# Kernel tuning notes

Hardware: AMD Instinct MI355X
Metric: run time of the kernel (lower is better)

The kernel has to match this reference:

```python
import jax, jax.numpy as jnp
import numpy as np

N, E = 40000, 640000
D, H, DK = 128, 8, 16   # out_dim, n_heads, d_k = D // H
T, R = 3, 4             # num node types, num relation types


def setup_inputs() -> dict:
    key = jax.random.key(0)
    ks = jax.random.split(key, 16)
    glorot = lambda k, shape, fan: jax.random.normal(k, shape, jnp.float32) * np.sqrt(2.0 / fan)
    inp = {
        'node_inp': jax.random.normal(ks[0], (N, D), jnp.float32),
        'node_type': jax.random.randint(ks[1], (N,), 0, T),
        'edge_index': jax.random.randint(ks[2], (2, E), 0, N),
        'edge_type': jax.random.randint(ks[3], (E,), 0, R),
        'node_position': jax.random.randint(ks[4], (N,), 0, N),
        # per-node-type Linear weights, stored [T, in, out] (y = x @ W + b)
        'Kw': glorot(ks[5], (T, D, D), 2 * D), 'Kb': jnp.zeros((T, D), jnp.float32),
        'Qw': glorot(ks[6], (T, D, D), 2 * D), 'Qb': jnp.zeros((T, D), jnp.float32),
        'Vw': glorot(ks[7], (T, D, D), 2 * D), 'Vb': jnp.zeros((T, D), jnp.float32),
        'Aw': glorot(ks[8], (T, D, D), 2 * D), 'Ab': jnp.zeros((T, D), jnp.float32),
        'relation_pri': jnp.ones((T, R, T, H), jnp.float32),
        'relation_att': glorot(ks[9], (R, H, DK, DK), 2 * DK),
        'relation_msg': glorot(ks[10], (R, H, DK, DK), 2 * DK),
        'relation_s2u': glorot(ks[11], (D, D), 2 * D),
        'skip': jnp.ones((T,), jnp.float32),
    }
    return inp


def reference(node_inp, node_type, edge_index, edge_type, node_position,
              Kw, Kb, Qw, Qb, Vw, Vb, Aw, Ab,
              relation_pri, relation_att, relation_msg, relation_s2u, skip):
    n = node_inp.shape[0]
    src, tgt = edge_index[0], edge_index[1]  # j (source), i (target)
    ar = jnp.arange(n)

    # per-type K/Q/V projections for every node: [T, N, D], then select own type
    k_all = jnp.einsum('nd,tdo->tno', node_inp, Kw) + Kb[:, None, :]
    q_all = jnp.einsum('nd,tdo->tno', node_inp, Qw) + Qb[:, None, :]
    v_all = jnp.einsum('nd,tdo->tno', node_inp, Vw) + Vb[:, None, :]
    k_node = k_all[node_type, ar]
    q_node = q_all[node_type, ar]
    v_node = v_all[node_type, ar]

    k_j = k_node[src].reshape(-1, H, DK)
    v_j = v_node[src].reshape(-1, H, DK)
    q_i = q_node[tgt].reshape(-1, H, DK)

    # per-relation attention / message transforms (select per edge relation)
    k_t = jnp.zeros_like(k_j)
    v_t = jnp.zeros_like(v_j)
    for r in range(R):
        sel = (edge_type == r)[:, None, None]
        k_t = jnp.where(sel, jnp.einsum('ehd,hdf->ehf', k_j, relation_att[r]), k_t)
        v_t = jnp.where(sel, jnp.einsum('ehd,hdf->ehf', v_j, relation_msg[r]), v_t)

    st, tt = node_type[src], node_type[tgt]
    pri = relation_pri[tt, edge_type, st]                       # [E, H]
    att_raw = (q_i * k_t).sum(-1) * pri / np.sqrt(DK)           # [E, H]

    # scatter-softmax over edges sharing the same target node
    m = jax.ops.segment_max(att_raw, tgt, num_segments=n)
    m = jnp.where(jnp.isfinite(m), m, 0.0)
    ex = jnp.exp(att_raw - m[tgt])
    den = jax.ops.segment_sum(ex, tgt, num_segments=n)
    att = ex / (den[tgt] + 1e-16)

    msg = (v_t * att[:, :, None]).reshape(-1, D)
    aggr = jax.ops.segment_sum(msg, tgt, num_segments=n)        # scatter-add

    # speaker information: edges with edge_type==0, message from target rep to source index
    sp_in = v_all[1][tgt]                                       # v_linears[1](node_inp[edge_index_i])
    sp_msg = sp_in @ relation_s2u                               # [E, D]
    drop_idx = jnp.where(edge_type == 0, src, n)                # out-of-range -> dropped
    speaker_info = jnp.zeros((n, D), node_inp.dtype).at[drop_idx].set(sp_msg, mode='drop')

    aggr = jax.nn.gelu(aggr + speaker_info, approximate=False)

    # target-specific aggregation with per-type learnable skip (dropout=eval identity)
    a_all = jnp.einsum('no,tof->tnf', aggr, Aw) + Ab[:, None, :]
    a_node = a_all[node_type, ar]
    alpha = jax.nn.sigmoid(skip)[node_type][:, None]
    return a_node * alpha + node_inp * (1.0 - alpha)
```

## Files before the change

kernel.cpp:

```cpp
#include <hip/hip_runtime.h>
#include <hip/hip_bf16.h>
#include <math.h>

#define ND 128
#define NH 8
#define DKK 16
#define NT 3
#define NR 4
#define NB 8
#define NMAT 12
#define SCB 4096

typedef unsigned short ushort_t;
typedef __bf16 bf16_t;
typedef bf16_t bf16x8 __attribute__((ext_vector_type(8)));
typedef float f32x4 __attribute__((ext_vector_type(4)));

__device__ __forceinline__ float bf2f(unsigned short u) {
    union { unsigned int i; float f; } v; v.i = ((unsigned int)u) << 16; return v.f;
}
__device__ __forceinline__ unsigned short f2bf(float f) {
    union { float f; unsigned int i; } v; v.f = f;
    unsigned int x = v.i;
    unsigned int lsb = (x >> 16) & 1u;
    x += 0x7fffu + lsb;
    return (unsigned short)(x >> 16);
}
__device__ __forceinline__ unsigned int pk2(float a, float b) {
    return (unsigned int)f2bf(a) | ((unsigned int)f2bf(b) << 16);
}
__device__ __forceinline__ void load_bf8(const ushort_t* p, float* o) {
    uint4 u = *reinterpret_cast<const uint4*>(p);
    o[0]=bf2f(u.x & 0xffff); o[1]=bf2f(u.x >> 16);
    o[2]=bf2f(u.y & 0xffff); o[3]=bf2f(u.y >> 16);
    o[4]=bf2f(u.z & 0xffff); o[5]=bf2f(u.z >> 16);
    o[6]=bf2f(u.w & 0xffff); o[7]=bf2f(u.w >> 16);
}
__device__ __forceinline__ bf16x8 as_bf16x8(uint4 u) {
    union { uint4 u; bf16x8 v; } c; c.u = u; return c.v;
}


__global__ void k_zero(int n, int* offs, int* winner) {
    int i = blockIdx.x * 256 + threadIdx.x;
    if (i < n) { offs[i] = 0; winner[i] = -1; }
}

__global__ void k_count(int e, const int* src, const int* tgt, const int* etype,
                        int* offs, int* winner, int* rank) {
    int i = blockIdx.x * 256 + threadIdx.x;
    if (i < e) {
        rank[i] = atomicAdd(&offs[tgt[i]], 1);
        if (etype[i] == 0) atomicMax(&winner[src[i]], i);
    }
}


__global__ void k_scanA(int n, const int* offs, const int* ntype, int* bsum4) {
    __shared__ int red[256];
    __shared__ int tr[256][3];
    int b = blockIdx.x, tid = threadIdx.x;
    int base = b * SCB + tid * 16;
    int s = 0, c0 = 0, c1 = 0, c2 = 0;
    #pragma unroll
    for (int i = 0; i < 16; i++) {
        int idx = base + i;
        if (idx < n) {
            s += offs[idx];
            int t = ntype[idx];
            c0 += (t == 0); c1 += (t == 1); c2 += (t == 2);
        }
    }
    red[tid] = s; tr[tid][0] = c0; tr[tid][1] = c1; tr[tid][2] = c2;
    __syncthreads();
    for (int d = 128; d > 0; d >>= 1) {
        if (tid < d) {
            red[tid] += red[tid + d];
            tr[tid][0] += tr[tid + d][0];
            tr[tid][1] += tr[tid + d][1];
            tr[tid][2] += tr[tid + d][2];
        }
        __syncthreads();
    }
    if (tid == 0) {
        bsum4[b * 4]     = red[0];
        bsum4[b * 4 + 1] = tr[0][0];
        bsum4[b * 4 + 2] = tr[0][1];
        bsum4[b * 4 + 3] = tr[0][2];
    }
}

__global__ void k_scanB(int nb, const int* bsum4, int* boff4, int* tcnt, int* tstart) {
    if (threadIdx.x == 0) {
        int run = 0, r0 = 0, r1 = 0, r2 = 0;
        for (int b = 0; b < nb; b++) {
            boff4[b * 4]     = run;
            boff4[b * 4 + 1] = r0;
            boff4[b * 4 + 2] = r1;
            boff4[b * 4 + 3] = r2;
            run += bsum4[b * 4];
            r0  += bsum4[b * 4 + 1];
            r1  += bsum4[b * 4 + 2];
            r2  += bsum4[b * 4 + 3];
        }
        tcnt[0] = r0; tcnt[1] = r1; tcnt[2] = r2;
        tstart[0] = 0; tstart[1] = r0; tstart[2] = r0 + r1;
    }
}

__global__ void k_scanC(int n, int* offs, const int* ntype, const int* boff4,
                        const int* tstart, int* order) {
    __shared__ int red[256];
    __shared__ int tr[256][3];
    int b = blockIdx.x, tid = threadIdx.x;
    int base = b * SCB + tid * 16;
    int v[16]; signed char ty[16];
    int s = 0, c0 = 0, c1 = 0, c2 = 0;
    #pragma unroll
    for (int i = 0; i < 16; i++) {
        int idx = base + i;
        v[i] = (idx < n) ? offs[idx] : 0;
        s += v[i];
        int t = (idx < n) ? ntype[idx] : -1;
        ty[i] = (signed char)t;
        c0 += (t == 0); c1 += (t == 1); c2 += (t == 2);
    }
    red[tid] = s; tr[tid][0] = c0; tr[tid][1] = c1; tr[tid][2] = c2;
    __syncthreads();
    for (int d = 1; d < 256; d <<= 1) {
        int vv = (tid >= d) ? red[tid - d] : 0;
        int w0 = (tid >= d) ? tr[tid - d][0] : 0;
        int w1 = (tid >= d) ? tr[tid - d][1] : 0;
        int w2 = (tid >= d) ? tr[tid - d][2] : 0;
        __syncthreads();
        red[tid] += vv; tr[tid][0] += w0; tr[tid][1] += w1; tr[tid][2] += w2;
        __syncthreads();
    }
    int run = boff4[b * 4] + red[tid] - s;
    int p0 = tstart[0] + boff4[b * 4 + 1] + tr[tid][0] - c0;
    int p1 = tstart[1] + boff4[b * 4 + 2] + tr[tid][1] - c1;
    int p2 = tstart[2] + boff4[b * 4 + 3] + tr[tid][2] - c2;
    #pragma unroll
    for (int i = 0; i < 16; i++) {
        int idx = base + i;
        if (idx < n) {
            offs[idx] = run; run += v[i];
            int t = ty[i];
            if (t == 0)      order[p0++] = idx;
            else if (t == 1) order[p1++] = idx;
            else             order[p2++] = idx;
        }
    }
    if (base <= n && n < base + 16) offs[n] = run;
}

__global__ void k_scatter(int e, const int* src, const int* tgt, const int* etype,
                          const int* ntype, const int* offs, const int* rank,
                          int* eord, int mode) {
    int i = blockIdx.x * 256 + threadIdx.x;
    if (i < e) {
        int p = offs[tgt[i]] + rank[i];
        if (mode) {
            int s = src[i];
            eord[p] = (s * NR + etype[i]) | (ntype[s] << 28);
        } else {
            eord[p] = i;
        }
    }
}


__global__ void k_pack(const float* Qw, const float* Qb, const float* Kw, const float* Kb,
                       const float* Vw, const float* Vb, const float* Aw, const float* Ab,
                       const float* s2u, const float* r_att, const float* r_msg,
                       ushort_t* Wall, float* bcat) {
    int blk = blockIdx.x;
    int kb = blk & 3;
    int c = (blk >> 2) & 7;
    int tm = blk >> 5;
    int m = tm % NMAT, t = tm / NMAT;
    int lane = threadIdx.x;
    int nn = c * 16 + (lane & 15);
    int quad = lane >> 4;
    int k0 = kb * 32 + quad * 8;
    ushort_t* dst = Wall + (size_t)blk * 512 + lane * 8;

    if (m == 0 || m == 5 || m == 10 || m == 11) {
        const float* W; const float* B;
        if (m == 0)       { W = Qw + (size_t)t * ND * ND; B = Qb + t * ND; }
        else if (m == 5)  { W = Vw + (size_t)ND * ND;     B = Vb + ND; }
        else if (m == 10) { W = Aw + (size_t)t * ND * ND; B = Ab + t * ND; }
        else              { W = s2u;                      B = nullptr; }
        #pragma unroll
        for (int j = 0; j < 8; j++) dst[j] = f2bf(W[(size_t)(k0 + j) * ND + nn]);
        if (kb == 0 && quad == 0)
            bcat[(t * NMAT + m) * ND + nn] = B ? B[nn] : 0.f;
    } else {
        int r = (m <= 4) ? (m - 1) : (m - 6);
        const float* W0 = (m <= 4) ? Kw : Vw;
        const float* B0 = (m <= 4) ? Kb : Vb;
        const float* Wr = (m <= 4) ? r_att : r_msg;
        int h = c, f = lane & 15;
        float wcol[16];
        #pragma unroll
        for (int jj = 0; jj < 16; jj++)
            wcol[jj] = Wr[(((size_t)r * NH + h) * DKK + jj) * DKK + f];
        #pragma unroll
        for (int j = 0; j < 8; j++) {
            const float* row = W0 + ((size_t)t * ND + (k0 + j)) * ND + h * DKK;
            float s = 0.f;
            #pragma unroll
            for (int jj = 0; jj < 16; jj++) s += row[jj] * wcol[jj];
            dst[j] = f2bf(s);
        }
        if (kb == 0 && quad == 0) {
            const float* brow = B0 + t * ND + h * DKK;
            float sb = 0.f;
            #pragma unroll
            for (int jj = 0; jj < 16; jj++) sb += brow[jj] * wcol[jj];
            bcat[(t * NMAT + m) * ND + nn] = sb;
        }
    }
}

__global__ void __launch_bounds__(256) k_projm(
    int n, const float* x_in, const int* order,
    const int* tcnt, const int* tstart,
    const ushort_t* Wall, const float* bcat,
    int m0, int nm,
    ushort_t* out_qn, ushort_t* out_kt, ushort_t* out_v1, ushort_t* out_vt)
{
    __shared__ __align__(16) ushort_t xs[4096];
    __shared__ int nodes[32];
    int b = blockIdx.x;
    int nb0 = (tcnt[0] + 31) >> 5, nb1 = (tcnt[1] + 31) >> 5, nb2 = (tcnt[2] + 31) >> 5;
    int t, lb;
    if (b < nb0)                  { t = 0; lb = b; }
    else if (b < nb0 + nb1)       { t = 1; lb = b - nb0; }
    else if (b < nb0 + nb1 + nb2) { t = 2; lb = b - nb0 - nb1; }
    else return;
    int segoff = lb * 32;
    int cnt = min(32, tcnt[t] - segoff);
    int segbase = tstart[t] + segoff;
    int tid = threadIdx.x;
    if (tid < 32) nodes[tid] = (tid < cnt) ? order[segbase + tid] : -1;
    __syncthreads();
    {
        int row = tid >> 3;
        int d0 = (tid & 7) * 16;
        int rt = row >> 4, rl = row & 15;
        int kb = d0 >> 5, q0 = (d0 >> 3) & 3;
        uint4 c0, c1;
        if (row < cnt) {
            const float4* xp4 = (const float4*)(x_in + (size_t)nodes[row] * ND + d0);
            float4 a = xp4[0], b2 = xp4[1], c2 = xp4[2], d4 = xp4[3];
            c0.x = pk2(a.x, a.y);   c0.y = pk2(a.z, a.w);
            c0.z = pk2(b2.x, b2.y); c0.w = pk2(b2.z, b2.w);
            c1.x = pk2(c2.x, c2.y); c1.y = pk2(c2.z, c2.w);
            c1.z = pk2(d4.x, d4.y); c1.w = pk2(d4.z, d4.w);
        } else {
            c0.x = c0.y = c0.z = c0.w = 0u;
            c1 = c0;
        }
        *(uint4*)&xs[((rt * 4 + kb) * 64 + q0 * 16 + rl) * 8]       = c0;
        *(uint4*)&xs[((rt * 4 + kb) * 64 + (q0 + 1) * 16 + rl) * 8] = c1;
    }
    __syncthreads();

    int w = tid >> 6, lane = tid & 63;
    int rt = w & 1;
    bf16x8 afr[4];
    #pragma unroll
    for (int kb = 0; kb < 4; kb++)
        afr[kb] = as_bf16x8(*(const uint4*)&xs[((rt * 4 + kb) * 64 + lane) * 8]);
    int nct = nm * 8;
    for (int ct = (w >> 1); ct < nct; ct += 2) {
        int m = m0 + (ct >> 3), c = ct & 7;
        const uint4* bp = (const uint4*)(Wall + ((((size_t)t * NMAT + m) * 8 + c) * 4) * 512);
        f32x4 acc = {0.f, 0.f, 0.f, 0.f};
        #pragma unroll
        for (int kb = 0; kb < 4; kb++) {
            bf16x8 bfr = as_bf16x8(bp[kb * 64 + lane]);
            acc = __builtin_amdgcn_mfma_f32_16x16x32_bf16(afr[kb], bfr, acc, 0, 0, 0);
        }
        int col = c * 16 + (lane & 15);
        float bias = bcat[(t * NMAT + m) * ND + col];
        int rbase = rt * 16 + (lane >> 4) * 4;
        #pragma unroll
        for (int r = 0; r < 4; r++) {
            int grow = rbase + r;
            if (grow >= cnt) continue;
            int node = nodes[grow];
            ushort_t val = f2bf(acc[r] + bias);
            if (m == 0)       out_qn[(size_t)node * ND + col] = val;
            else if (m <= 4)  out_kt[((size_t)node * NR + (m - 1)) * ND + col] = val;
            else if (m == 5)  out_v1[(size_t)node * ND + col] = val;
            else              out_vt[((size_t)node * NR + (m - 6)) * ND + col] = val;
        }
    }
}

__global__ void __launch_bounds__(256) k_projall(
    int n, const float* x_in, const int* order,
    const int* tcnt, const int* tstart,
    const ushort_t* Wall, const float* bcat,
    ushort_t* out_qn, ushort_t* out_kt, ushort_t* out_v1, ushort_t* out_vt)
{
    __shared__ __align__(16) ushort_t xs[4096];
    __shared__ int nodes[32];
    int b = blockIdx.x;
    int nb0 = (tcnt[0] + 31) >> 5, nb1 = (tcnt[1] + 31) >> 5, nb2 = (tcnt[2] + 31) >> 5;
    int t, lb;
    if (b < nb0)                  { t = 0; lb = b; }
    else if (b < nb0 + nb1)       { t = 1; lb = b - nb0; }
    else if (b < nb0 + nb1 + nb2) { t = 2; lb = b - nb0 - nb1; }
    else return;
    int segoff = lb * 32;
    int cnt = min(32, tcnt[t] - segoff);
    int segbase = tstart[t] + segoff;
    int tid = threadIdx.x;
    if (tid < 32) nodes[tid] = (tid < cnt) ? order[segbase + tid] : -1;
    __syncthreads();
    {
        int row = tid >> 3;
        int d0 = (tid & 7) * 16;
        int rt = row >> 4, rl = row & 15;
        int kb = d0 >> 5, q0 = (d0 >> 3) & 3;
        uint4 c0, c1;
        if (row < cnt) {
            const float4* xp4 = (const float4*)(x_in + (size_t)nodes[row] * ND + d0);
            float4 a = xp4[0], b2 = xp4[1], c2 = xp4[2], d4 = xp4[3];
            c0.x = pk2(a.x, a.y);   c0.y = pk2(a.z, a.w);
            c0.z = pk2(b2.x, b2.y); c0.w = pk2(b2.z, b2.w);
            c1.x = pk2(c2.x, c2.y); c1.y = pk2(c2.z, c2.w);
            c1.z = pk2(d4.x, d4.y); c1.w = pk2(d4.z, d4.w);
        } else {
            c0.x = c0.y = c0.z = c0.w = 0u;
            c1 = c0;
        }
        *(uint4*)&xs[((rt * 4 + kb) * 64 + q0 * 16 + rl) * 8]       = c0;
        *(uint4*)&xs[((rt * 4 + kb) * 64 + (q0 + 1) * 16 + rl) * 8] = c1;
    }
    __syncthreads();

    int w = tid >> 6, lane = tid & 63;
    int rt = w & 1;
    bf16x8 afr[4];
    #pragma unroll
    for (int kb = 0; kb < 4; kb++)
        afr[kb] = as_bf16x8(*(const uint4*)&xs[((rt * 4 + kb) * 64 + lane) * 8]);
    for (int ct = (w >> 1); ct < 80; ct += 2) {
        int m = ct >> 3, c = ct & 7;
        const uint4* bp = (const uint4*)(Wall + ((((size_t)t * NMAT + m) * 8 + c) * 4) * 512);
        f32x4 acc = {0.f, 0.f, 0.f, 0.f};
        #pragma unroll
        for (int kb = 0; kb < 4; kb++) {
            bf16x8 bfr = as_bf16x8(bp[kb * 64 + lane]);
            acc = __builtin_amdgcn_mfma_f32_16x16x32_bf16(afr[kb], bfr, acc, 0, 0, 0);
        }
        int col = c * 16 + (lane & 15);
        float bias = bcat[(t * NMAT + m) * ND + col];
        int rbase = rt * 16 + (lane >> 4) * 4;
        #pragma unroll
        for (int r = 0; r < 4; r++) {
            int grow = rbase + r;
            if (grow >= cnt) continue;
            int node = nodes[grow];
            ushort_t val = f2bf(acc[r] + bias);
            if (m == 0)       out_qn[(size_t)node * ND + col] = val;
            else if (m <= 4)  out_kt[((size_t)node * NR + (m - 1)) * ND + col] = val;
            else if (m == 5)  out_v1[(size_t)node * ND + col] = val;
            else              out_vt[((size_t)node * NR + (m - 6)) * ND + col] = val;
        }
    }
}

__global__ void __launch_bounds__(256) k_flash(
    int n, const int* off, const int* srp, const int* ntype,
    const ushort_t* qn, const ushort_t* kt, const ushort_t* vt,
    const float* r_pri, float* aggr)
{
    int wv = threadIdx.x >> 6, lane = threadIdx.x & 63;
    int i = blockIdx.x * 4 + wv;
    if (i >= n) return;
    int h = lane & 7, slot = lane >> 3;
    int hA = lane >> 3;
    int tt = ntype[i];
    float qf[16];
    load_bf8(qn + (size_t)i * ND + h * DKK, qf);
    load_bf8(qn + (size_t)i * ND + h * DKK + 8, qf + 8);
    const float* prib = r_pri + (size_t)(tt * NR * NT) * NH + h;
    int d0 = off[i], d1 = off[i + 1];
    float m = -3.0e38f, den = 0.f;
    float acc0 = 0.f, acc1 = 0.f;
    for (int p0 = d0; p0 < d1; p0 += 8) {
        int p = p0 + slot;
        bool live = (p < d1);
        int sp = live ? srp[p] : 0;
        int sr = sp & 0x0fffffff;
        int st = ((unsigned int)sp) >> 28;
        int r = sr & (NR - 1);
        float kf[16];
        const ushort_t* kp = kt + (size_t)sr * ND + h * DKK;
        load_bf8(kp, kf);
        load_bf8(kp + 8, kf + 8);
        float a = 0.f;
        #pragma unroll
        for (int f = 0; f < 16; f++) a += qf[f] * kf[f];
        float pri = prib[(r * NT + st) * NH];
        float logit = fminf(fmaxf(a * pri * 0.25f, -1.0e4f), 1.0e4f);
        if (!live) logit = -3.0e38f;
        float cm = logit;
        #pragma unroll
        for (int d = 8; d < 64; d <<= 1) cm = fmaxf(cm, __shfl_xor(cm, d, 64));
        float mnew = fmaxf(m, cm);
        float w = live ? expf(logit - mnew) : 0.f;
        float ws = w;
        #pragma unroll
        for (int d = 8; d < 64; d <<= 1) ws += __shfl_xor(ws, d, 64);
        float scale = expf(m - mnew);
        den = den * scale + ws;
        m = mnew;
        float scaleA = __shfl(scale, hA, 64);
        acc0 *= scaleA; acc1 *= scaleA;
        #pragma unroll
        for (int s = 0; s < 8; s++) {
            if (p0 + s < d1) {
                int srcl = s * 8 + hA;
                int srb  = __shfl(sr, srcl, 64);
                float wb = __shfl(w, srcl, 64);
                unsigned int u = *reinterpret_cast<const unsigned int*>(
                    vt + (size_t)srb * ND + lane * 2);
                acc0 += wb * bf2f(u & 0xffff);
                acc1 += wb * bf2f(u >> 16);
            }
        }
    }
    float denA = __shfl(den, hA, 64);
    float inv = 1.f / (denA + 1e-16f);
    float2 o; o.x = acc0 * inv; o.y = acc1 * inv;
    *reinterpret_cast<float2*>(aggr + (size_t)i * ND + lane * 2) = o;
}

__global__ void __launch_bounds__(256) k_sfinal(
    int n, const float* x_in, const int* order, const int* tcnt, const int* tstart,
    const int* winner, const int* tgt, const ushort_t* v1b,
    const ushort_t* Wall, const float* bcat, const float* skip,
    const float* aggr, float* out)
{
    __shared__ __align__(16) float xf[32 * 132];
    __shared__ __align__(16) ushort_t xs[4096];
    __shared__ int nodes[32];
    __shared__ int wsrc[32];
    int b = blockIdx.x;
    int nb0 = (tcnt[0] + 31) >> 5, nb1 = (tcnt[1] + 31) >> 5, nb2 = (tcnt[2] + 31) >> 5;
    int t, lb;
    if (b < nb0)                  { t = 0; lb = b; }
    else if (b < nb0 + nb1)       { t = 1; lb = b - nb0; }
    else if (b < nb0 + nb1 + nb2) { t = 2; lb = b - nb0 - nb1; }
    else return;
    int segoff = lb * 32;
    int cnt = min(32, tcnt[t] - segoff);
    int segbase = tstart[t] + segoff;
    int tid = threadIdx.x;
    if (tid < 32) {
        int nd = (tid < cnt) ? order[segbase + tid] : -1;
        nodes[tid] = nd;
        int wi = (nd >= 0) ? winner[nd] : -1;
        wsrc[tid] = (wi >= 0) ? tgt[wi] : -1;
    }
    __syncthreads();
    {
        int row = tid >> 3;
        int d0 = (tid & 7) * 16;
        int rt = row >> 4, rl = row & 15;
        int kb = d0 >> 5, q0 = (d0 >> 3) & 3;
        uint4 c0, c1;
        int s = (row < cnt) ? wsrc[row] : -1;
        if (s >= 0) {
            const uint4* vp = (const uint4*)(v1b + (size_t)s * ND + d0);
            c0 = vp[0]; c1 = vp[1];
        } else { c0.x = c0.y = c0.z = c0.w = 0u; c1 = c0; }
        *(uint4*)&xs[((rt * 4 + kb) * 64 + q0 * 16 + rl) * 8]       = c0;
        *(uint4*)&xs[((rt * 4 + kb) * 64 + (q0 + 1) * 16 + rl) * 8] = c1;
    }
    __syncthreads();
    int w = tid >> 6, lane = tid & 63;
    int rt = w & 1;
    {
        bf16x8 afr[4];
        #pragma unroll
        for (int kb = 0; kb < 4; kb++)
            afr[kb] = as_bf16x8(*(const uint4*)&xs[((rt * 4 + kb) * 64 + lane) * 8]);
        for (int ct = (w >> 1); ct < 8; ct += 2) {
            const uint4* bp = (const uint4*)(Wall + (((size_t)11 * 8 + ct) * 4) * 512);
            f32x4 acc = {0.f, 0.f, 0.f, 0.f};
            #pragma unroll
            for (int kb = 0; kb < 4; kb++) {
                bf16x8 bfr = as_bf16x8(bp[kb * 64 + lane]);
                acc = __builtin_amdgcn_mfma_f32_16x16x32_bf16(afr[kb], bfr, acc, 0, 0, 0);
            }
            int col = ct * 16 + (lane & 15);
            int rbase = rt * 16 + (lane >> 4) * 4;
            #pragma unroll
            for (int r = 0; r < 4; r++) {
// ... 231 lines not shown
    float den = 0.f;
    for (int p = d0; p < d1; p++) den += expf(att[(size_t)sorted[p] * NH + h] - mref);
    mb[id] = mh;
    db[id] = den;
}

__global__ void k_norm(int e, const int* tgt, const ushort_t* mb, const float* db, float* att) {
    int id = blockIdx.x * 256 + threadIdx.x;
    if (id >= e * NH) return;
    int ee = id >> 3, h = id & 7;
    int t = tgt[ee];
    float w = expf(att[id] - bf2f(mb[t * NH + h])) / (db[t * NH + h] + 1e-16f);
    att[id] = w;
}

__global__ void k_aggr(int n, const int* off, const int* sorted, const int* src, const int* etype,
                       const ushort_t* vn, const float* r_msg, const float* att, float* aggr) {
    int wv = threadIdx.x >> 6, lane = threadIdx.x & 63;
    int i = blockIdx.x * 4 + wv;
    if (i >= n) return;
    int h = lane >> 3, f0 = (lane & 7) * 2;
    int d0 = off[i], d1 = off[i + 1];
    float acc0 = 0.f, acc1 = 0.f;
    for (int p = d0; p < d1; p++) {
        int ee = sorted[p];
        int s = src[ee], r = etype[ee];
        float w = att[(size_t)ee * NH + h];
        float vj[16];
        load_bf8(vn + (size_t)s * ND + h * DKK, vj);
        load_bf8(vn + (size_t)s * ND + h * DKK + 8, vj + 8);
        const float* Wm = r_msg + (size_t)(r * NH + h) * DKK * DKK + f0;
        float a0 = 0.f, a1 = 0.f;
        #pragma unroll
        for (int d = 0; d < 16; d++) {
            a0 += vj[d] * Wm[d * 16];
            a1 += vj[d] * Wm[d * 16 + 1];
        }
        acc0 += w * a0; acc1 += w * a1;
    }
    aggr[(size_t)i * ND + h * DKK + f0]     = acc0;
    aggr[(size_t)i * ND + h * DKK + f0 + 1] = acc1;
}

__global__ void k_spk(int n, const int* winner, const int* tgt, const ushort_t* v1,
                      const float* s2u, float* aggr) {
    __shared__ float xs[NB][ND];
    __shared__ int wn[NB];
    int tid = threadIdx.x;
    int base = blockIdx.x * NB;
    int cnt = min(NB, n - base);
    if (tid < cnt) wn[tid] = winner[base + tid];
    __syncthreads();
    for (int j = 0; j < cnt; j++) {
        int w = wn[j];
        xs[j][tid] = (w >= 0) ? bf2f(v1[(size_t)tgt[w] * ND + tid]) : 0.f;
    }
    __syncthreads();
    float acc[NB];
    #pragma unroll
    for (int j = 0; j < NB; j++) acc[j] = 0.f;
    const float* Wp = s2u + tid;
    for (int d = 0; d < ND; d++) {
        float w = Wp[(size_t)d * ND];
        #pragma unroll
        for (int j = 0; j < NB; j++) acc[j] += xs[j][d] * w;
    }
    for (int j = 0; j < cnt; j++) {
        size_t idx = (size_t)(base + j) * ND + tid;
        float g = aggr[idx] + acc[j];
        g = 0.5f * g * (1.f + erff(g * 0.70710678118f));
        aggr[idx] = g;
    }
}

__global__ void k_final(int n, const float* x_in, const int* ntype, const int* order,
                        const float* Aw, const float* Ab, const float* skip,
                        const float* aggr, float* out) {
    __shared__ float xs[NB][ND];
    __shared__ int nodes[NB];
    __shared__ int types[NB];
    int tid = threadIdx.x;
    int base = blockIdx.x * NB;
    int cnt = min(NB, n - base);
    if (tid < cnt) { int nd = order[base + tid]; nodes[tid] = nd; types[tid] = ntype[nd]; }
    __syncthreads();
    for (int j = 0; j < cnt; j++) xs[j][tid] = aggr[(size_t)nodes[j] * ND + tid];
    __syncthreads();
    bool uni = (types[0] == types[cnt - 1]);
    if (uni) {
        int t = types[0];
        float bias = Ab[t * ND + tid];
        float acc[NB];
        #pragma unroll
        for (int j = 0; j < NB; j++) acc[j] = bias;
        const float* Wp = Aw + (size_t)t * ND * ND + tid;
        for (int d = 0; d < ND; d++) {
            float w = Wp[(size_t)d * ND];
            #pragma unroll
            for (int j = 0; j < NB; j++) acc[j] += xs[j][d] * w;
        }
        float alpha = 1.f / (1.f + expf(-skip[t]));
        for (int j = 0; j < cnt; j++) {
            float xin = x_in[(size_t)nodes[j] * ND + tid];
            out[(size_t)nodes[j] * ND + tid] = acc[j] * alpha + xin * (1.f - alpha);
        }
    } else {
        for (int j = 0; j < cnt; j++) {
            int t = types[j];
            float acc = Ab[t * ND + tid];
            const float* Wp = Aw + (size_t)t * ND * ND + tid;
            for (int d = 0; d < ND; d++) acc += xs[j][d] * Wp[(size_t)d * ND];
            float alpha = 1.f / (1.f + expf(-skip[t]));
            float xin = x_in[(size_t)nodes[j] * ND + tid];
            out[(size_t)nodes[j] * ND + tid] = acc * alpha + xin * (1.f - alpha);
        }
    }
}

extern "C" void kernel_launch(void* const* d_in, const int* in_sizes, int n_in,
                              void* d_out, int out_size, void* d_ws, size_t ws_size,
                              hipStream_t stream) {
    const float* node_inp = (const float*)d_in[0];
    const int* node_type  = (const int*)d_in[1];
    const int* edge_index = (const int*)d_in[2];
    const int* edge_type  = (const int*)d_in[3];
    const float* Kw = (const float*)d_in[5];
    const float* Kb = (const float*)d_in[6];
    const float* Qw = (const float*)d_in[7];
    const float* Qb = (const float*)d_in[8];
    const float* Vw = (const float*)d_in[9];
    const float* Vb = (const float*)d_in[10];
    const float* Aw = (const float*)d_in[11];
    const float* Ab = (const float*)d_in[12];
    const float* r_pri = (const float*)d_in[13];
    const float* r_att = (const float*)d_in[14];
    const float* r_msg = (const float*)d_in[15];
    const float* s2u   = (const float*)d_in[16];
    const float* skip  = (const float*)d_in[17];

    int n = in_sizes[1];
    int e = in_sizes[3];
    const int* srcp = edge_index;
    const int* tgtp = edge_index + e;

    char* wsp = (char*)d_ws;
    size_t woff = 0;
    auto alloc = [&](size_t b) { void* p = wsp + woff; woff += (b + 255) & ~(size_t)255; return p; };

    int* offs     = (int*)alloc((size_t)(n + 1) * 4);
    int* winner   = (int*)alloc((size_t)n * 4);
    int* order    = (int*)alloc((size_t)n * 4);
    int* tcnt     = (int*)alloc(16);
    int* tstart   = (int*)alloc(16);
    int* bsum4    = (int*)alloc(4096);
    int* boff4    = (int*)alloc(4096);
    int* eord     = (int*)alloc((size_t)e * 4);
    ushort_t* mb  = (ushort_t*)alloc((size_t)n * NH * 2);
    float* db     = (float*)alloc((size_t)n * NH * 4);
    ushort_t* v1b = (ushort_t*)alloc((size_t)n * ND * 2);
    float* att    = (float*)alloc((size_t)e * NH * 4);
    size_t commonEnd = woff;

    int* rank = (int*)att;

    woff = commonEnd;
    ushort_t* WallB = (ushort_t*)alloc((size_t)NT * NMAT * 8 * 4 * 512 * 2);
    float* bcatB    = (float*)alloc((size_t)NT * NMAT * ND * 4);
    char* F         = (char*)alloc((size_t)n * 1536);
    size_t fastEnd = woff;

    woff = commonEnd;
    ushort_t* WallA = (ushort_t*)alloc((size_t)NT * NMAT * 8 * 4 * 512 * 2);
    float* bcatA    = (float*)alloc((size_t)NT * NMAT * ND * 4);
    ushort_t* qnA   = (ushort_t*)alloc((size_t)n * ND * 2);
    ushort_t* ktA   = (ushort_t*)alloc((size_t)n * NR * ND * 2);
    ushort_t* vtA   = (ushort_t*)alloc((size_t)n * NR * ND * 2);
    size_t tierAEnd = woff;
    float* aggrA = (float*)att;

    int gn = (n + 255) / 256;
    int ge = (e + 255) / 256;
    int nbscan = n / SCB + 1;
    int gproj = (n + 31) / 32 + NT;

    int tierA = (ws_size >= tierAEnd) && ((size_t)e * NH >= (size_t)n * ND);
    int fast  = (ws_size >= fastEnd);

    k_zero<<<gn, 256, 0, stream>>>(n, offs, winner);
    k_count<<<ge, 256, 0, stream>>>(e, srcp, tgtp, edge_type, offs, winner, rank);
    k_scanA<<<nbscan, 256, 0, stream>>>(n, offs, node_type, bsum4);
    k_scanB<<<1, 64, 0, stream>>>(nbscan, bsum4, boff4, tcnt, tstart);
    k_scanC<<<nbscan, 256, 0, stream>>>(n, offs, node_type, boff4, tstart, order);
    k_scatter<<<ge, 256, 0, stream>>>(e, srcp, tgtp, edge_type, node_type, offs, rank,
                                      eord, (tierA || fast) ? 1 : 0);

    if (tierA) {
        k_pack<<<NT * NMAT * 8 * 4, 64, 0, stream>>>(Qw, Qb, Kw, Kb, Vw, Vb, Aw, Ab,
                                                     s2u, r_att, r_msg, WallA, bcatA);
        k_projall<<<gproj, 256, 0, stream>>>(n, node_inp, order, tcnt, tstart, WallA, bcatA,
                                             qnA, ktA, v1b, vtA);
        k_flash<<<(n + 3) / 4, 256, 0, stream>>>(n, offs, eord, node_type,
                                                 qnA, ktA, vtA, r_pri, aggrA);
        k_sfinal<<<gproj, 256, 0, stream>>>(n, node_inp, order, tcnt, tstart,
                                            winner, tgtp, v1b, WallA, bcatA, skip,
                                            aggrA, (float*)d_out);
    } else if (fast) {
        ushort_t* qn  = (ushort_t*)F;
        ushort_t* kt  = (ushort_t*)(F + (size_t)n * 256);
        ushort_t* vt  = (ushort_t*)F;
        float* aggr   = (float*)(F + (size_t)n * 1024);

        k_pack<<<NT * NMAT * 8 * 4, 64, 0, stream>>>(Qw, Qb, Kw, Kb, Vw, Vb, Aw, Ab,
                                                     s2u, r_att, r_msg, WallB, bcatB);
        k_projm<<<gproj, 256, 0, stream>>>(n, node_inp, order, tcnt, tstart, WallB, bcatB,
                                           0, 6, qn, kt, v1b, (ushort_t*)nullptr);
        k_attmd<<<(n + 3) / 4, 256, 0, stream>>>(n, offs, eord, node_type,
                                                 qn, kt, r_pri, att, mb, db);
        k_projm<<<gproj, 256, 0, stream>>>(n, node_inp, order, tcnt, tstart, WallB, bcatB,
                                           6, 4, (ushort_t*)nullptr, (ushort_t*)nullptr,
                                           (ushort_t*)nullptr, vt);
        k_aggr_fast<<<(n + 3) / 4, 256, 0, stream>>>(n, offs, eord, vt, att, mb, db, aggr);
        k_sfinal<<<gproj, 256, 0, stream>>>(n, node_inp, order, tcnt, tstart,
                                            winner, tgtp, v1b, WallB, bcatB, skip,
                                            aggr, (float*)d_out);
    } else {
        woff = commonEnd;
        ushort_t* vn  = (ushort_t*)alloc((size_t)n * ND * 2);
        char* regA    = (char*)alloc((size_t)n * ND * 2 * 2);
        ushort_t* kn  = (ushort_t*)regA;
        ushort_t* qn  = (ushort_t*)(regA + (size_t)n * ND * 2);
        float* aggr   = (float*)regA;

        k_proj<<<(n + NB - 1) / NB, 128, 0, stream>>>(n, node_inp, node_type, order,
                                                      Kw, Kb, Qw, Qb, Vw, Vb, kn, qn, vn, v1b);
        k_att<<<(e * NH + 255) / 256, 256, 0, stream>>>(e, srcp, tgtp, edge_type, node_type,
                                                        kn, qn, r_att, r_pri, att);
        k_mden<<<(n * NH + 255) / 256, 256, 0, stream>>>(n, offs, eord, att, mb, db);
        k_norm<<<(e * NH + 255) / 256, 256, 0, stream>>>(e, tgtp, mb, db, att);
        k_aggr<<<(n + 3) / 4, 256, 0, stream>>>(n, offs, eord, srcp, edge_type, vn, r_msg, att, aggr);
        k_spk<<<(n + NB - 1) / NB, 128, 0, stream>>>(n, winner, tgtp, v1b, s2u, aggr);
        k_final<<<(n + NB - 1) / NB, 128, 0, stream>>>(n, node_inp, node_type, order,
                                                       Aw, Ab, skip, aggr, (float*)d_out);
    }
}
```

Before: 323.8 us.

## Fuse edge counting into projection kernel and split node-type and offset scans

```diff
diff --git a/kernel.cpp b/kernel.cpp
--- a/kernel.cpp
+++ b/kernel.cpp
@@ -47,35 +47,32 @@
 }
 
 __global__ void k_count(int e, const int* src, const int* tgt, const int* etype,
-                        int* offs, int* winner, int* rank) {
+                        int* cnts, int* winner, int* rank) {
     int i = blockIdx.x * 256 + threadIdx.x;
     if (i < e) {
-        rank[i] = atomicAdd(&offs[tgt[i]], 1);
+        rank[i] = atomicAdd(&cnts[tgt[i]], 1);
         if (etype[i] == 0) atomicMax(&winner[src[i]], i);
     }
 }
 
 
-__global__ void k_scanA(int n, const int* offs, const int* ntype, int* bsum4) {
-    __shared__ int red[256];
+__global__ void k_nscanA(int n, const int* ntype, int* nb4) {
     __shared__ int tr[256][3];
     int b = blockIdx.x, tid = threadIdx.x;
     int base = b * SCB + tid * 16;
-    int s = 0, c0 = 0, c1 = 0, c2 = 0;
+    int c0 = 0, c1 = 0, c2 = 0;
     #pragma unroll
     for (int i = 0; i < 16; i++) {
         int idx = base + i;
         if (idx < n) {
-            s += offs[idx];
             int t = ntype[idx];
             c0 += (t == 0); c1 += (t == 1); c2 += (t == 2);
         }
     }
-    red[tid] = s; tr[tid][0] = c0; tr[tid][1] = c1; tr[tid][2] = c2;
+    tr[tid][0] = c0; tr[tid][1] = c1; tr[tid][2] = c2;
     __syncthreads();
     for (int d = 128; d > 0; d >>= 1) {
         if (tid < d) {
-            red[tid] += red[tid + d];
             tr[tid][0] += tr[tid + d][0];
             tr[tid][1] += tr[tid + d][1];
             tr[tid][2] += tr[tid + d][2];
@@ -83,73 +80,119 @@
         __syncthreads();
     }
     if (tid == 0) {
-        bsum4[b * 4]     = red[0];
-        bsum4[b * 4 + 1] = tr[0][0];
-        bsum4[b * 4 + 2] = tr[0][1];
-        bsum4[b * 4 + 3] = tr[0][2];
-    }
-}
-
-__global__ void k_scanB(int nb, const int* bsum4, int* boff4, int* tcnt, int* tstart) {
+        nb4[b * 4]     = tr[0][0];
+        nb4[b * 4 + 1] = tr[0][1];
+        nb4[b * 4 + 2] = tr[0][2];
+    }
+}
+
+__global__ void k_nscanB(int nb, const int* nb4, int* nboff4, int* tcnt, int* tstart) {
     if (threadIdx.x == 0) {
-        int run = 0, r0 = 0, r1 = 0, r2 = 0;
+        int r0 = 0, r1 = 0, r2 = 0;
         for (int b = 0; b < nb; b++) {
-            boff4[b * 4]     = run;
-            boff4[b * 4 + 1] = r0;
-            boff4[b * 4 + 2] = r1;
-            boff4[b * 4 + 3] = r2;
-            run += bsum4[b * 4];
-            r0  += bsum4[b * 4 + 1];
-            r1  += bsum4[b * 4 + 2];
-            r2  += bsum4[b * 4 + 3];
+            nboff4[b * 4]     = r0;
+            nboff4[b * 4 + 1] = r1;
+            nboff4[b * 4 + 2] = r2;
+            r0 += nb4[b * 4];
+            r1 += nb4[b * 4 + 1];
+            r2 += nb4[b * 4 + 2];
         }
         tcnt[0] = r0; tcnt[1] = r1; tcnt[2] = r2;
         tstart[0] = 0; tstart[1] = r0; tstart[2] = r0 + r1;
     }
 }
 
-__global__ void k_scanC(int n, int* offs, const int* ntype, const int* boff4,
-                        const int* tstart, int* order) {
-    __shared__ int red[256];
+__global__ void k_nscanC(int n, const int* ntype, const int* nboff4,
+                         const int* tstart, int* order) {
     __shared__ int tr[256][3];
     int b = blockIdx.x, tid = threadIdx.x;
     int base = b * SCB + tid * 16;
-    int v[16]; signed char ty[16];
-    int s = 0, c0 = 0, c1 = 0, c2 = 0;
+    signed char ty[16];
+    int c0 = 0, c1 = 0, c2 = 0;
+    #pragma unroll
+    for (int i = 0; i < 16; i++) {
+        int idx = base + i;
+        int t = (idx < n) ? ntype[idx] : -1;
+        ty[i] = (signed char)t;
+        c0 += (t == 0); c1 += (t == 1); c2 += (t == 2);
+    }
+    tr[tid][0] = c0; tr[tid][1] = c1; tr[tid][2] = c2;
+    __syncthreads();
+    for (int d = 1; d < 256; d <<= 1) {
+        int w0 = (tid >= d) ? tr[tid - d][0] : 0;
+        int w1 = (tid >= d) ? tr[tid - d][1] : 0;
+        int w2 = (tid >= d) ? tr[tid - d][2] : 0;
+        __syncthreads();
+        tr[tid][0] += w0; tr[tid][1] += w1; tr[tid][2] += w2;
+        __syncthreads();
+    }
+    int p0 = tstart[0] + nboff4[b * 4]     + tr[tid][0] - c0;
+    int p1 = tstart[1] + nboff4[b * 4 + 1] + tr[tid][1] - c1;
+    int p2 = tstart[2] + nboff4[b * 4 + 2] + tr[tid][2] - c2;
+    #pragma unroll
+    for (int i = 0; i < 16; i++) {
+        int idx = base + i;
+        if (idx < n) {
+            int t = ty[i];
+            if (t == 0)      order[p0++] = idx;
+            else if (t == 1) order[p1++] = idx;
+            else             order[p2++] = idx;
+        }
+    }
+}
+
+
+__global__ void k_oscanA(int n, const int* offs, int* ob) {
+    __shared__ int red[256];
+    int b = blockIdx.x, tid = threadIdx.x;
+    int base = b * SCB + tid * 16;
+    int s = 0;
+    #pragma unroll
+    for (int i = 0; i < 16; i++) {
+        int idx = base + i;
+        if (idx < n) s += offs[idx];
+    }
+    red[tid] = s;
+    __syncthreads();
+    for (int d = 128; d > 0; d >>= 1) {
+        if (tid < d) red[tid] += red[tid + d];
+        __syncthreads();
+    }
+    if (tid == 0) ob[b] = red[0];
+}
+
+__global__ void k_oscanB(int nb, const int* ob, int* oboff) {
+    if (threadIdx.x == 0) {
+        int run = 0;
+        for (int b = 0; b < nb; b++) { oboff[b] = run; run += ob[b]; }
+    }
+}
+
+__global__ void k_oscanC(int n, int* offs, const int* oboff) {
+    __shared__ int red[256];
+    int b = blockIdx.x, tid = threadIdx.x;
+    int base = b * SCB + tid * 16;
+    int v[16];
+    int s = 0;
     #pragma unroll
     for (int i = 0; i < 16; i++) {
         int idx = base + i;
         v[i] = (idx < n) ? offs[idx] : 0;
         s += v[i];
-        int t = (idx < n) ? ntype[idx] : -1;
-        ty[i] = (signed char)t;
-        c0 += (t == 0); c1 += (t == 1); c2 += (t == 2);
-    }
-    red[tid] = s; tr[tid][0] = c0; tr[tid][1] = c1; tr[tid][2] = c2;
+    }
+    red[tid] = s;
     __syncthreads();
     for (int d = 1; d < 256; d <<= 1) {
         int vv = (tid >= d) ? red[tid - d] : 0;
-        int w0 = (tid >= d) ? tr[tid - d][0] : 0;
-        int w1 = (tid >= d) ? tr[tid - d][1] : 0;
-        int w2 = (tid >= d) ? tr[tid - d][2] : 0;
         __syncthreads();
-        red[tid] += vv; tr[tid][0] += w0; tr[tid][1] += w1; tr[tid][2] += w2;
+        red[tid] += vv;
         __syncthreads();
     }
-    int run = boff4[b * 4] + red[tid] - s;
-    int p0 = tstart[0] + boff4[b * 4 + 1] + tr[tid][0] - c0;
-    int p1 = tstart[1] + boff4[b * 4 + 2] + tr[tid][1] - c1;
-    int p2 = tstart[2] + boff4[b * 4 + 3] + tr[tid][2] - c2;
+    int run = oboff[b] + red[tid] - s;
     #pragma unroll
     for (int i = 0; i < 16; i++) {
         int idx = base + i;
-        if (idx < n) {
-            offs[idx] = run; run += v[i];
-            int t = ty[i];
-            if (t == 0)      order[p0++] = idx;
-            else if (t == 1) order[p1++] = idx;
-            else             order[p2++] = idx;
-        }
+        if (idx < n) { offs[idx] = run; run += v[i]; }
     }
     if (base <= n && n < base + 16) offs[n] = run;
 }
@@ -219,6 +262,94 @@
             #pragma unroll
             for (int jj = 0; jj < 16; jj++) sb += brow[jj] * wcol[jj];
             bcat[(t * NMAT + m) * ND + nn] = sb;
+        }
+    }
+}
+
+__global__ void __launch_bounds__(256) k_fuse(
+    int n, int e, int gproj, int gtot,
+    const int* src, const int* tgt, const int* etype,
+    int* cnts, int* winner, int* rank,
+    const float* x_in, const int* order, const int* tcnt, const int* tstart,
+    const ushort_t* Wall, const float* bcat,
+    ushort_t* out_qn, ushort_t* out_kt, ushort_t* out_v1, ushort_t* out_vt)
+{
+    __shared__ __align__(16) ushort_t xs[4096];
+    __shared__ int nodes[32];
+    int bid = blockIdx.x;
+    int pb  = (int)(((long long)bid * gproj) / gtot);
+    int pb1 = (int)(((long long)(bid + 1) * gproj) / gtot);
+    if (pb1 == pb) {
+        int i = (bid - pb) * 256 + threadIdx.x;
+        if (i < e) {
+            rank[i] = atomicAdd(&cnts[tgt[i]], 1);
+            if (etype[i] == 0) atomicMax(&winner[src[i]], i);
+        }
+        return;
+    }
+    int b = pb;
+    int nb0 = (tcnt[0] + 31) >> 5, nb1 = (tcnt[1] + 31) >> 5, nb2 = (tcnt[2] + 31) >> 5;
+    int t, lb;
+    if (b < nb0)                  { t = 0; lb = b; }
+    else if (b < nb0 + nb1)       { t = 1; lb = b - nb0; }
+    else if (b < nb0 + nb1 + nb2) { t = 2; lb = b - nb0 - nb1; }
+    else return;
+    int segoff = lb * 32;
+    int cnt = min(32, tcnt[t] - segoff);
+    int segbase = tstart[t] + segoff;
+    int tid = threadIdx.x;
+    if (tid < 32) nodes[tid] = (tid < cnt) ? order[segbase + tid] : -1;
+    __syncthreads();
+    {
+        int row = tid >> 3;
+        int d0 = (tid & 7) * 16;
+        int rt = row >> 4, rl = row & 15;
+        int kb = d0 >> 5, q0 = (d0 >> 3) & 3;
+        uint4 c0, c1;
+        if (row < cnt) {
+            const float4* xp4 = (const float4*)(x_in + (size_t)nodes[row] * ND + d0);
+            float4 a = xp4[0], b2 = xp4[1], c2 = xp4[2], d4 = xp4[3];
+            c0.x = pk2(a.x, a.y);   c0.y = pk2(a.z, a.w);
+            c0.z = pk2(b2.x, b2.y); c0.w = pk2(b2.z, b2.w);
+            c1.x = pk2(c2.x, c2.y); c1.y = pk2(c2.z, c2.w);
+            c1.z = pk2(d4.x, d4.y); c1.w = pk2(d4.z, d4.w);
+        } else {
+            c0.x = c0.y = c0.z = c0.w = 0u;
+            c1 = c0;
+        }
+        *(uint4*)&xs[((rt * 4 + kb) * 64 + q0 * 16 + rl) * 8]       = c0;
+        *(uint4*)&xs[((rt * 4 + kb) * 64 + (q0 + 1) * 16 + rl) * 8] = c1;
+    }
+    __syncthreads();
+
+    int w = tid >> 6, lane = tid & 63;
+    int rt = w & 1;
+    bf16x8 afr[4];
+    #pragma unroll
+    for (int kb = 0; kb < 4; kb++)
+        afr[kb] = as_bf16x8(*(const uint4*)&xs[((rt * 4 + kb) * 64 + lane) * 8]);
+    for (int ct = (w >> 1); ct < 80; ct += 2) {
+        int m = ct >> 3, c = ct & 7;
+        const uint4* bp = (const uint4*)(Wall + ((((size_t)t * NMAT + m) * 8 + c) * 4) * 512);
+        f32x4 acc = {0.f, 0.f, 0.f, 0.f};
+        #pragma unroll
+        for (int kb = 0; kb < 4; kb++) {
+            bf16x8 bfr = as_bf16x8(bp[kb * 64 + lane]);
+            acc = __builtin_amdgcn_mfma_f32_16x16x32_bf16(afr[kb], bfr, acc, 0, 0, 0);
+        }
+        int col = c * 16 + (lane & 15);
+        float bias = bcat[(t * NMAT + m) * ND + col];
+        int rbase = rt * 16 + (lane >> 4) * 4;
+        #pragma unroll
+        for (int r = 0; r < 4; r++) {
+            int grow = rbase + r;
+            if (grow >= cnt) continue;
+            int node = nodes[grow];
+            ushort_t val = f2bf(acc[r] + bias);
+            if (m == 0)       out_qn[(size_t)node * ND + col] = val;
+            else if (m <= 4)  out_kt[((size_t)node * NR + (m - 1)) * ND + col] = val;
+            else if (m == 5)  out_v1[(size_t)node * ND + col] = val;
+            else              out_vt[((size_t)node * NR + (m - 6)) * ND + col] = val;
         }
     }
 }
@@ -276,81 +407,6 @@
     int nct = nm * 8;
     for (int ct = (w >> 1); ct < nct; ct += 2) {
         int m = m0 + (ct >> 3), c = ct & 7;
-        const uint4* bp = (const uint4*)(Wall + ((((size_t)t * NMAT + m) * 8 + c) * 4) * 512);
-        f32x4 acc = {0.f, 0.f, 0.f, 0.f};
-        #pragma unroll
-        for (int kb = 0; kb < 4; kb++) {
-            bf16x8 bfr = as_bf16x8(bp[kb * 64 + lane]);
-            acc = __builtin_amdgcn_mfma_f32_16x16x32_bf16(afr[kb], bfr, acc, 0, 0, 0);
-        }
-        int col = c * 16 + (lane & 15);
-        float bias = bcat[(t * NMAT + m) * ND + col];
-        int rbase = rt * 16 + (lane >> 4) * 4;
-        #pragma unroll
-        for (int r = 0; r < 4; r++) {
-            int grow = rbase + r;
-            if (grow >= cnt) continue;
-            int node = nodes[grow];
-            ushort_t val = f2bf(acc[r] + bias);
-            if (m == 0)       out_qn[(size_t)node * ND + col] = val;
-            else if (m <= 4)  out_kt[((size_t)node * NR + (m - 1)) * ND + col] = val;
-            else if (m == 5)  out_v1[(size_t)node * ND + col] = val;
-            else              out_vt[((size_t)node * NR + (m - 6)) * ND + col] = val;
-        }
-    }
-}
-
-__global__ void __launch_bounds__(256) k_projall(
-    int n, const float* x_in, const int* order,
-    const int* tcnt, const int* tstart,
-    const ushort_t* Wall, const float* bcat,
-    ushort_t* out_qn, ushort_t* out_kt, ushort_t* out_v1, ushort_t* out_vt)
-{
-    __shared__ __align__(16) ushort_t xs[4096];
-    __shared__ int nodes[32];
-    int b = blockIdx.x;
-    int nb0 = (tcnt[0] + 31) >> 5, nb1 = (tcnt[1] + 31) >> 5, nb2 = (tcnt[2] + 31) >> 5;
-    int t, lb;
-    if (b < nb0)                  { t = 0; lb = b; }
-    else if (b < nb0 + nb1)       { t = 1; lb = b - nb0; }
-    else if (b < nb0 + nb1 + nb2) { t = 2; lb = b - nb0 - nb1; }
-    else return;
-    int segoff = lb * 32;
-    int cnt = min(32, tcnt[t] - segoff);
-    int segbase = tstart[t] + segoff;
-    int tid = threadIdx.x;
-    if (tid < 32) nodes[tid] = (tid < cnt) ? order[segbase + tid] : -1;
-    __syncthreads();
-    {
-        int row = tid >> 3;
-        int d0 = (tid & 7) * 16;
-        int rt = row >> 4, rl = row & 15;
-        int kb = d0 >> 5, q0 = (d0 >> 3) & 3;
-        uint4 c0, c1;
-        if (row < cnt) {
-            const float4* xp4 = (const float4*)(x_in + (size_t)nodes[row] * ND + d0);
-            float4 a = xp4[0], b2 = xp4[1], c2 = xp4[2], d4 = xp4[3];
-            c0.x = pk2(a.x, a.y);   c0.y = pk2(a.z, a.w);
-            c0.z = pk2(b2.x, b2.y); c0.w = pk2(b2.z, b2.w);
-            c1.x = pk2(c2.x, c2.y); c1.y = pk2(c2.z, c2.w);
-            c1.z = pk2(d4.x, d4.y); c1.w = pk2(d4.z, d4.w);
-        } else {
-            c0.x = c0.y = c0.z = c0.w = 0u;
-            c1 = c0;
-        }
-        *(uint4*)&xs[((rt * 4 + kb) * 64 + q0 * 16 + rl) * 8]       = c0;
-        *(uint4*)&xs[((rt * 4 + kb) * 64 + (q0 + 1) * 16 + rl) * 8] = c1;
-    }
-    __syncthreads();
-
-    int w = tid >> 6, lane = tid & 63;
-    int rt = w & 1;
-    bf16x8 afr[4];
-    #pragma unroll
-    for (int kb = 0; kb < 4; kb++)
-        afr[kb] = as_bf16x8(*(const uint4*)&xs[((rt * 4 + kb) * 64 + lane) * 8]);
-    for (int ct = (w >> 1); ct < 80; ct += 2) {
-        int m = ct >> 3, c = ct & 7;
         const uint4* bp = (const uint4*)(Wall + ((((size_t)t * NMAT + m) * 8 + c) * 4) * 512);
         f32x4 acc = {0.f, 0.f, 0.f, 0.f};
         #pragma unroll
@@ -888,8 +944,10 @@
     int* order    = (int*)alloc((size_t)n * 4);
     int* tcnt     = (int*)alloc(16);
     int* tstart   = (int*)alloc(16);
-    int* bsum4    = (int*)alloc(4096);
-    int* boff4    = (int*)alloc(4096);
+    int* nb4      = (int*)alloc(4096);
+    int* nboff4   = (int*)alloc(4096);
+    int* ob       = (int*)alloc(4096);
+    int* oboff    = (int*)alloc(4096);
     int* eord     = (int*)alloc((size_t)e * 4);
     ushort_t* mb  = (ushort_t*)alloc((size_t)n * NH * 2);
     float* db     = (float*)alloc((size_t)n * NH * 4);
@@ -923,18 +981,23 @@
     int fast  = (ws_size >= fastEnd);
 
     k_zero<<<gn, 256, 0, stream>>>(n, offs, winner);
-    k_count<<<ge, 256, 0, stream>>>(e, srcp, tgtp, edge_type, offs, winner, rank);
-    k_scanA<<<nbscan, 256, 0, stream>>>(n, offs, node_type, bsum4);
-    k_scanB<<<1, 64, 0, stream>>>(nbscan, bsum4, boff4, tcnt, tstart);
-    k_scanC<<<nbscan, 256, 0, stream>>>(n, offs, node_type, boff4, tstart, order);
-    k_scatter<<<ge, 256, 0, stream>>>(e, srcp, tgtp, edge_type, node_type, offs, rank,
-                                      eord, (tierA || fast) ? 1 : 0);
+    k_nscanA<<<nbscan, 256, 0, stream>>>(n, node_type, nb4);
+    k_nscanB<<<1, 64, 0, stream>>>(nbscan, nb4, nboff4, tcnt, tstart);
+    k_nscanC<<<nbscan, 256, 0, stream>>>(n, node_type, nboff4, tstart, order);
 
     if (tierA) {
         k_pack<<<NT * NMAT * 8 * 4, 64, 0, stream>>>(Qw, Qb, Kw, Kb, Vw, Vb, Aw, Ab,
                                                      s2u, r_att, r_msg, WallA, bcatA);
-        k_projall<<<gproj, 256, 0, stream>>>(n, node_inp, order, tcnt, tstart, WallA, bcatA,
-                                             qnA, ktA, v1b, vtA);
+        int gtot = gproj + ge;
+        k_fuse<<<gtot, 256, 0, stream>>>(n, e, gproj, gtot, srcp, tgtp, edge_type,
+                                         offs, winner, rank,
+                                         node_inp, order, tcnt, tstart, WallA, bcatA,
+                                         qnA, ktA, v1b, vtA);
+        k_oscanA<<<nbscan, 256, 0, stream>>>(n, offs, ob);
+        k_oscanB<<<1, 64, 0, stream>>>(nbscan, ob, oboff);
+        k_oscanC<<<nbscan, 256, 0, stream>>>(n, offs, oboff);
+        k_scatter<<<ge, 256, 0, stream>>>(e, srcp, tgtp, edge_type, node_type,
+                                          offs, rank, eord, 1);
         k_flash<<<(n + 3) / 4, 256, 0, stream>>>(n, offs, eord, node_type,
                                                  qnA, ktA, vtA, r_pri, aggrA);
         k_sfinal<<<gproj, 256, 0, stream>>>(n, node_inp, order, tcnt, tstart,
@@ -946,6 +1009,12 @@
         ushort_t* vt  = (ushort_t*)F;
         float* aggr   = (float*)(F + (size_t)n * 1024);
 
+        k_count<<<ge, 256, 0, stream>>>(e, srcp, tgtp, edge_type, offs, winner, rank);
+        k_oscanA<<<nbscan, 256, 0, stream>>>(n, offs, ob);
+        k_oscanB<<<1, 64, 0, stream>>>(nbscan, ob, oboff);
+        k_oscanC<<<nbscan, 256, 0, stream>>>(n, offs, oboff);
+        k_scatter<<<ge, 256, 0, stream>>>(e, srcp, tgtp, edge_type, node_type,
+                                          offs, rank, eord, 1);
         k_pack<<<NT * NMAT * 8 * 4, 64, 0, stream>>>(Qw, Qb, Kw, Kb, Vw, Vb, Aw, Ab,
                                                      s2u, r_att, r_msg, WallB, bcatB);
         k_projm<<<gproj, 256, 0, stream>>>(n, node_inp, order, tcnt, tstart, WallB, bcatB,
@@ -967,6 +1036,12 @@
         ushort_t* qn  = (ushort_t*)(regA + (size_t)n * ND * 2);
         float* aggr   = (float*)regA;
 
+        k_count<<<ge, 256, 0, stream>>>(e, srcp, tgtp, edge_type, offs, winner, rank);
+        k_oscanA<<<nbscan, 256, 0, stream>>>(n, offs, ob);
+        k_oscanB<<<1, 64, 0, stream>>>(nbscan, ob, oboff);
+        k_oscanC<<<nbscan, 256, 0, stream>>>(n, offs, oboff);
+        k_scatter<<<ge, 256, 0, stream>>>(e, srcp, tgtp, edge_type, node_type,
+                                          offs, rank, eord, 0);
         k_proj<<<(n + NB - 1) / NB, 128, 0, stream>>>(n, node_inp, node_type, order,
                                                       Kw, Kb, Qw, Qb, Vw, Vb, kn, qn, vn, v1b);
         k_att<<<(e * NH + 255) / 256, 256, 0, stream>>>(e, srcp, tgtp, edge_type, node_type,
```

Result: no change. 329.9 us (+1.9%).
